# Kernel tuning notes

Measured on AMD Instinct MI355X. Metric: run time of the kernel, lower is better.

The kernel has to match this reference:

```python
import jax, jax.numpy as jnp
import numpy as np

TEACHER_TEMP = 0.07
STUDENT_TEMP = 0.1
N_SK_ITERS = 3
SK_EPS = 1e-8
KOLEO_EPS = 1e-8


def l2norm(x, eps=1e-12):
    # matches F.normalize(p=2, dim=-1): x / max(||x||, eps)
    n = jnp.linalg.norm(x, axis=-1, keepdims=True)
    return x / jnp.maximum(n, eps)


def sinkhorn_knopp(logits, temp):
    # logits: [M, K] -> doubly-stochastic-ish Q: [M, K]
    M = logits / temp
    M = M - jnp.max(M)
    Q = jnp.exp(M).T  # [K, M]
    for _ in range(N_SK_ITERS):
        Q = Q / (jnp.sum(Q, axis=1, keepdims=True) + SK_EPS)  # normalize over samples
        Q = Q / (jnp.sum(Q, axis=0, keepdims=True) + SK_EPS)  # normalize over prototypes
    return Q.T


def koleo_loss(x):
    # DINOv2 KoLeo: -mean(log(distance to nearest neighbor))
    x = l2norm(x, KOLEO_EPS)
    n = x.shape[0]
    dots = x @ x.T  # [K, K]
    dots = jnp.where(jnp.eye(n, dtype=bool), -1.0, dots)  # exclude self (fill diag with -1)
    nn_idx = jnp.argmax(dots, axis=1)
    d = jnp.linalg.norm(x - x[nn_idx], axis=-1)
    return -jnp.mean(jnp.log(d + KOLEO_EPS))


def setup_inputs() -> dict:
    key = jax.random.key(0)
    k1, k2, k3, k4 = jax.random.split(key, 4)
    B, N, D, K = 8, 1024, 768, 8192
    return {
        "teacher_patch_tokens": jax.random.normal(k1, (B, N, D), jnp.float32),
        "student_patch_tokens": jax.random.normal(k2, (B, N, D), jnp.float32),
        "token_masks": jax.random.randint(k3, (B, N), 0, 2) > 0,
        "proto_weight": jax.random.normal(k4, (K, D), jnp.float32) * 0.02,
    }


def reference(teacher_patch_tokens, student_patch_tokens, token_masks, proto_weight):
    B, N, D = teacher_patch_tokens.shape
    K = proto_weight.shape[0]

    t = l2norm(teacher_patch_tokens)  # [B,N,D]
    s = l2norm(student_patch_tokens)

    # prototype bank = bias-free linear: logits = x @ W^T
    t_logits = jnp.einsum('bnd,kd->bnk', t, proto_weight)  # [B,N,K]

    # Sinkhorn-Knopp targets (no grad)
    Q = jax.lax.stop_gradient(
        sinkhorn_knopp(t_logits.reshape(B * N, K), TEACHER_TEMP)
    ).reshape(B, N, K)

    t_logp = jax.nn.log_softmax(t_logits / TEACHER_TEMP, axis=-1)
    teacher_proto_loss = -jnp.sum(Q * t_logp) / (B * N)

    koleo = koleo_loss(l2norm(proto_weight))

    # Student cross-entropy on masked tokens. Dense-masked formulation:
    # computes the same mean over masked positions as boolean indexing.
    s_logits = jnp.einsum('bnd,kd->bnk', s, proto_weight)
    s_logp = jax.nn.log_softmax(s_logits / STUDENT_TEMP, axis=-1)
    per_token = -jnp.sum(Q * s_logp, axis=-1)  # [B,N]
    m = token_masks.astype(per_token.dtype)
    clustering_loss = jnp.sum(per_token * m) / jnp.maximum(jnp.sum(m), 1.0)

    return jnp.stack([clustering_loss, teacher_proto_loss, koleo])
```

## Files before the change

kernel.cpp:

```cpp
#include <hip/hip_runtime.h>
#include <stdint.h>

typedef unsigned short u16;
typedef __bf16 bf16x8 __attribute__((ext_vector_type(8)));
typedef float f32x4 __attribute__((ext_vector_type(4)));
typedef unsigned short u16x8 __attribute__((ext_vector_type(8)));
typedef unsigned short u16x4 __attribute__((ext_vector_type(4)));

#define SK_EPS 1e-8f
#define S_T 20.60992915555662f
#define S_S 14.426950408889634f
#define INV_TT 14.285714285714286f
#define INV_TS 10.0f

__device__ __forceinline__ float b2f(u16 u){ return __uint_as_float(((unsigned)u)<<16); }
__device__ __forceinline__ u16 f2b(float f){
  unsigned u = __float_as_uint(f);
  u += 0x7FFFu + ((u>>16)&1u);
  return (u16)(u>>16);
}
__device__ __forceinline__ unsigned encf(float x){ unsigned u=__float_as_uint(x); return (u&0x80000000u)? ~u : (u|0x80000000u); }
__device__ __forceinline__ float decf(unsigned u){ return (u&0x80000000u)? __uint_as_float(u&0x7FFFFFFFu) : __uint_as_float(~u); }

__device__ __forceinline__ void gload16(const void* g, void* l){
  __builtin_amdgcn_global_load_lds((const __attribute__((address_space(1))) void*)g,
                                   (__attribute__((address_space(3))) void*)l, 16, 0, 0);
}

__global__ __launch_bounds__(192) void norm_cast(const float* __restrict__ in, u16* __restrict__ out, int donorm){
  int row = blockIdx.x, tid = threadIdx.x;
  const float4* p = (const float4*)(in + (size_t)row*768);
  float4 v = p[tid];
  float ss = v.x*v.x + v.y*v.y + v.z*v.z + v.w*v.w;
  #pragma unroll
  for (int off=1; off<64; off<<=1) ss += __shfl_xor(ss, off);
  __shared__ float smem[3];
  int wv = tid>>6;
  if ((tid&63)==0) smem[wv] = ss;
  __syncthreads();
  float tot = smem[0]+smem[1]+smem[2];
  float scale = donorm ? (1.0f/fmaxf(sqrtf(tot), 1e-12f)) : 1.0f;
  u16x4 o;
  o[0]=f2b(v.x*scale); o[1]=f2b(v.y*scale); o[2]=f2b(v.z*scale); o[3]=f2b(v.w*scale);
  *(u16x4*)(out + (size_t)row*768 + tid*4) = o;
}

template<int MODE>
__global__ __launch_bounds__(256) void gemm_bt(
    const u16* __restrict__ A, const u16* __restrict__ B, int Ndim, int Kd,
    u16* __restrict__ Cout,
    const u16* __restrict__ Tl, const float* __restrict__ a3, const float* __restrict__ b3,
    float* __restrict__ sexp, float* __restrict__ sdot, unsigned* __restrict__ maxd)
{
  __shared__ __align__(16) u16 As[128*64];
  __shared__ __align__(16) u16 Bs[128*64];
  int tid = threadIdx.x, lane = tid & 63, wave = tid >> 6;
  int wr = wave >> 1, wc = wave & 1;
  int nbn = Ndim >> 7;
  int nwg = gridDim.x, cpx = nwg >> 3;
  int bid = blockIdx.x;
  int swz = (bid & 7)*cpx + (bid >> 3);
  int tm = swz / nbn, tn = swz % nbn;
  int m0 = tm<<7, n0 = tn<<7;

  const f32x4 fzero = {0.f,0.f,0.f,0.f};
  f32x4 acc[4][4];
  #pragma unroll
  for (int i=0;i<4;++i)
    #pragma unroll
    for (int j=0;j<4;++j) acc[i][j] = fzero;

  int srcRow = lane>>3;
  int srcCol = (((lane&7) ^ (lane>>3)) << 3);

  int nkt = Kd>>6;
  for (int kt=0; kt<nkt; ++kt){
    if (kt) __syncthreads();
    int k0 = kt<<6;
    #pragma unroll
    for (int c=0;c<4;++c){
      int chunk = (wave<<2)+c;
      int row = (chunk<<3) + srcRow;
      gload16(A + (size_t)(m0+row)*Kd + k0 + srcCol, (void*)(As + (chunk<<9)));
      gload16(B + (size_t)(n0+row)*Kd + k0 + srcCol, (void*)(Bs + (chunk<<9)));
    }
    asm volatile("s_waitcnt vmcnt(0)" ::: "memory");
    __syncthreads();
    #pragma unroll
    for (int ks=0; ks<2; ++ks){
      bf16x8 af[4], bfr[4];
      #pragma unroll
      for (int f=0; f<4; ++f){
        int rowA = (wr<<6)+(f<<4)+(lane&15);
        int idxA = ((rowA<<6) + (ks<<5) + ((lane>>4)<<3)) ^ ((lane&7)<<3);
        af[f] = *(const bf16x8*)(const void*)(As + idxA);
        int rowB = (wc<<6)+(f<<4)+(lane&15);
        int idxB = ((rowB<<6) + (ks<<5) + ((lane>>4)<<3)) ^ ((lane&7)<<3);
        bfr[f] = *(const bf16x8*)(const void*)(Bs + idxB);
      }
      #pragma unroll
      for (int fm=0;fm<4;++fm)
        #pragma unroll
        for (int fn=0;fn<4;++fn)
          acc[fm][fn] = __builtin_amdgcn_mfma_f32_16x16x32_bf16(af[fm], bfr[fn], acc[fm][fn], 0,0,0);
    }
  }

  if constexpr (MODE == 0){
    #pragma unroll
    for (int fm=0;fm<4;++fm)
      #pragma unroll
      for (int j=0;j<4;++j){
        size_t gr = (size_t)(m0 + (wr<<6)+(fm<<4)+((lane>>4)<<2)+j);
        #pragma unroll
        for (int fn=0;fn<4;++fn){
          int cl = (wc<<6)+(fn<<4)+(lane&15);
          Cout[gr*(size_t)Ndim + n0+cl] = f2b(acc[fm][fn][j]);
        }
      }
  } else if constexpr (MODE == 1){
    #pragma unroll
    for (int fm=0;fm<4;++fm)
      #pragma unroll
      for (int j=0;j<4;++j){
        size_t gr = (size_t)(m0 + (wr<<6)+(fm<<4)+((lane>>4)<<2)+j);
        float sx=0.f, sd=0.f;
        #pragma unroll
        for (int fn=0;fn<4;++fn){
          int cl = (wc<<6)+(fn<<4)+(lane&15);
          size_t gc = (size_t)(n0+cl);
          float v = acc[fm][fn][j];
          float tl = b2f(Tl[gr*(size_t)Ndim + gc]);
          sx += exp2f(v*S_S);
          sd += exp2f(tl*S_T)*a3[gc]*v;
        }
        #pragma unroll
        for (int off=1; off<16; off<<=1){ sx += __shfl_xor(sx,off); sd += __shfl_xor(sd,off); }
        if ((lane&15)==0){
          atomicAdd(&sexp[gr], sx);
          atomicAdd(&sdot[gr], b3[gr]*sd);
        }
      }
  } else {
    #pragma unroll
    for (int fm=0;fm<4;++fm)
      #pragma unroll
      for (int j=0;j<4;++j){
        size_t gr = (size_t)(m0 + (wr<<6)+(fm<<4)+((lane>>4)<<2)+j);
        float mx = -2.0f;
        #pragma unroll
        for (int fn=0;fn<4;++fn){
          int cl = (wc<<6)+(fn<<4)+(lane&15);
          size_t gc = (size_t)(n0+cl);
          float v = acc[fm][fn][j];
          if (gr != gc) mx = fmaxf(mx, v);
        }
        #pragma unroll
        for (int off=1; off<16; off<<=1) mx = fmaxf(mx, __shfl_xor(mx,off));
        if ((lane&15)==0) atomicMax(&maxd[gr], encf(mx));
      }
  }
}

__global__ __launch_bounds__(256) void sk_colsum(const u16* __restrict__ L, const float* __restrict__ bvec,
                                                 float* __restrict__ colOut, int Kc, int useb){
  int tid = threadIdx.x;
  int c0 = blockIdx.x*2048 + tid*8;
  int r0 = blockIdx.y*64;
  float acc[8] = {0.f,0.f,0.f,0.f,0.f,0.f,0.f,0.f};
  for (int r=r0; r<r0+64; ++r){
    u16x8 v = *(const u16x8*)(L + (size_t)r*Kc + c0);
    float bm = useb ? bvec[r] : 1.0f;
    #pragma unroll
    for (int i=0;i<8;++i) acc[i] += exp2f(b2f(v[i])*S_T)*bm;
  }
  #pragma unroll
  for (int i=0;i<8;++i) atomicAdd(&colOut[c0+i], acc[i]);
}

__global__ __launch_bounds__(256) void sk_rowsum(const u16* __restrict__ L, const float* __restrict__ avec,
    float* __restrict__ rowR, float* __restrict__ rowRE, float* __restrict__ rowT, int Kc, int mode){
  int m = blockIdx.x, tid = threadIdx.x;
  const u16* Lr = L + (size_t)m*Kc;
  float sR=0.f, sRE=0.f, sT=0.f;
  int nit = Kc/2048;
  for (int it=0; it<nit; ++it){
    int c = it*2048 + tid*8;
    u16x8 v = *(const u16x8*)(Lr + c);
    f32x4 alo = *(const f32x4*)(avec+c);
    f32x4 ahi = *(const f32x4*)(avec+c+4);
    #pragma unroll
    for (int i=0;i<8;++i){
      float l = b2f(v[i]);
      float E = exp2f(l*S_T);
      float a = (i<4)? alo[i] : ahi[i-4];
      float Ea = E*a;
      sR += Ea;
      if (mode&1) sRE += E;
      if (mode&2) sT += Ea*l;
    }
  }
  #pragma unroll
  for (int off=1; off<64; off<<=1){
    sR += __shfl_xor(sR,off);
    sRE += __shfl_xor(sRE,off);
    sT += __shfl_xor(sT,off);
  }
  __shared__ float red[3][4];
  int wv = tid>>6;
  if ((tid&63)==0){ red[0][wv]=sR; red[1][wv]=sRE; red[2][wv]=sT; }
  __syncthreads();
  if (tid==0){
    rowR[m] = red[0][0]+red[0][1]+red[0][2]+red[0][3];
    if (mode&1) rowRE[m] = red[1][0]+red[1][1]+red[1][2]+red[1][3];
    if (mode&2) rowT[m]  = red[2][0]+red[2][1]+red[2][2]+red[2][3];
  }
}

__global__ void upd_col(float* aV, float* colC, int K, int first){
  int k = blockIdx.x*256+threadIdx.x;
  if (k<K){
    float s = colC[k];
    float p = first ? 1.0f : aV[k];
    aV[k] = p/(p*s + SK_EPS);
    colC[k] = 0.0f;
  }
}
__global__ void upd_row(float* bV, const float* rowR, int M, int first){
  int m = blockIdx.x*256+threadIdx.x;
  if (m<M){
    float R = rowR[m];
    float p = first ? 1.0f : bV[m];
    bV[m] = p/(p*R + SK_EPS);
  }
}
__global__ void fin_rows(float* bV, const float* rowR, const float* rowRE, const float* rowT,
                         float* sumQ, float* ttok, int M){
  int m = blockIdx.x*256+threadIdx.x;
  if (m<M){
    float p = bV[m], R = rowR[m];
    float b3 = p/(p*R + SK_EPS);
    bV[m] = b3;
    float sq = b3*R;
    sumQ[m] = sq;
    ttok[m] = logf(rowRE[m])*sq - b3*rowT[m]*INV_TT;
  }
}

__global__ __launch_bounds__(1024) void finalize(const unsigned char* __restrict__ mask,
    const float* __restrict__ sexp, const float* __restrict__ sdot,
    const float* __restrict__ sumQ, const float* __restrict__ ttok,
    const unsigned* __restrict__ maxd, float* __restrict__ out, int M, int K){
  int tid = threadIdx.x;
  __shared__ int isBool;
  if (tid==0) isBool = 0;
  __syncthreads();
  int f = 0;
  for (int i=tid; i<M; i+=1024) if ((i&3) && mask[i]) f = 1;
  if (f) isBool = 1;
  __syncthreads();
  int ib = isBool;
  float cn=0.f, cc=0.f, ts=0.f, ks=0.f;
  for (int m=tid; m<M; m+=1024){
    int mk = ib ? (mask[m]!=0) : (((const int*)mask)[m]!=0);
    float pt = logf(sexp[m])*sumQ[m] - sdot[m]*INV_TS;
    if (mk){ cn += pt; cc += 1.0f; }
    ts += ttok[m];
  }
  for (int k=tid; k<K; k+=1024){
    float d = decf(maxd[k]);
    ks += logf(sqrtf(fmaxf(2.0f-2.0f*d, 0.0f)) + SK_EPS);
  }
  #pragma unroll
  for (int off=1; off<64; off<<=1){
    cn += __shfl_xor(cn,off); cc += __shfl_xor(cc,off);
    ts += __shfl_xor(ts,off); ks += __shfl_xor(ks,off);
  }
  __shared__ float red[4][16];
  int wv = tid>>6;
  if ((tid&63)==0){ red[0][wv]=cn; red[1][wv]=cc; red[2][wv]=ts; red[3][wv]=ks; }
  __syncthreads();
  if (tid==0){
    float CN=0,CC=0,TS=0,KS=0;
    for (int i=0;i<16;++i){ CN+=red[0][i]; CC+=red[1][i]; TS+=red[2][i]; KS+=red[3][i]; }
    out[0] = CN/fmaxf(CC,1.0f);
    out[1] = TS/(float)M;
    out[2] = -KS/(float)K;
  }
}

extern "C" void kernel_launch(void* const* d_in, const int* in_sizes, int n_in,
                              void* d_out, int out_size, void* d_ws, size_t ws_size,
                              hipStream_t stream){
  const float* teacher = (const float*)d_in[0];
  const float* student = (const float*)d_in[1];
  const unsigned char* mask = (const unsigned char*)d_in[2];
  const float* proto = (const float*)d_in[3];
  const int D = 768;
  const int M = in_sizes[0]/D;
  const int K = in_sizes[3]/D;
  float* out = (float*)d_out;

  char* ws = (char*)d_ws;
  size_t off = 0;
  auto alloc = [&](size_t bytes)->void*{ void* p = ws+off; off += (bytes+255)&~(size_t)255; return p; };
  u16* t_logits = (u16*)alloc((size_t)M*K*2);
  u16* t_hat    = (u16*)alloc((size_t)M*D*2);
  u16* s_hat    = (u16*)alloc((size_t)M*D*2);
  u16* w_bf     = (u16*)alloc((size_t)K*D*2);
  u16* w_hat    = (u16*)alloc((size_t)K*D*2);
  float* colC   = (float*)alloc((size_t)K*4);
  float* sexp   = (float*)alloc((size_t)M*4);
  float* sdot   = (float*)alloc((size_t)M*4);
  unsigned* maxd= (unsigned*)alloc((size_t)K*4);
  float* aV     = (float*)alloc((size_t)K*4);
  float* bV     = (float*)alloc((size_t)M*4);
  float* rowR   = (float*)alloc((size_t)M*4);
  float* rowRE  = (float*)alloc((size_t)M*4);
  float* rowT   = (float*)alloc((size_t)M*4);
  float* sumQ   = (float*)alloc((size_t)M*4);
  float* ttok   = (float*)alloc((size_t)M*4);

  hipMemsetAsync(colC, 0, (size_t)K*4, stream);
  hipMemsetAsync(sexp, 0, (size_t)M*4, stream);
  hipMemsetAsync(sdot, 0, (size_t)M*4, stream);
  hipMemsetAsync(maxd, 0, (size_t)K*4, stream);

  norm_cast<<<M, 192, 0, stream>>>(teacher, t_hat, 1);
  norm_cast<<<M, 192, 0, stream>>>(student, s_hat, 1);
  norm_cast<<<K, 192, 0, stream>>>(proto, w_bf, 0);
  norm_cast<<<K, 192, 0, stream>>>(proto, w_hat, 1);

  int nblk = (M/128)*(K/128);
  gemm_bt<0><<<nblk, 256, 0, stream>>>(t_hat, w_bf, K, D, t_logits,
                                       nullptr,nullptr,nullptr,nullptr,nullptr,nullptr);

  dim3 cgrid(K/2048, M/64);
  sk_colsum<<<cgrid, 256, 0, stream>>>(t_logits, nullptr, colC, K, 0);
  upd_col<<<(K+255)/256, 256, 0, stream>>>(aV, colC, K, 1);
  sk_rowsum<<<M, 256, 0, stream>>>(t_logits, aV, rowR, rowRE, rowT, K, 1);
  upd_row<<<(M+255)/256, 256, 0, stream>>>(bV, rowR, M, 1);
  sk_colsum<<<cgrid, 256, 0, stream>>>(t_logits, bV, colC, K, 1);
  upd_col<<<(K+255)/256, 256, 0, stream>>>(aV, colC, K, 0);
  sk_rowsum<<<M, 256, 0, stream>>>(t_logits, aV, rowR, rowRE, rowT, K, 0);
  upd_row<<<(M+255)/256, 256, 0, stream>>>(bV, rowR, M, 0);
  sk_colsum<<<cgrid, 256, 0, stream>>>(t_logits, bV, colC, K, 1);
  upd_col<<<(K+255)/256, 256, 0, stream>>>(aV, colC, K, 0);
  sk_rowsum<<<M, 256, 0, stream>>>(t_logits, aV, rowR, rowRE, rowT, K, 2);
  fin_rows<<<(M+255)/256, 256, 0, stream>>>(bV, rowR, rowRE, rowT, sumQ, ttok, M);

  gemm_bt<1><<<nblk, 256, 0, stream>>>(s_hat, w_bf, K, D, nullptr,
                                       t_logits, aV, bV, sexp, sdot, nullptr);
  gemm_bt<2><<<nblk, 256, 0, stream>>>(w_hat, w_hat, K, D, nullptr,
                                       nullptr,nullptr,nullptr,nullptr,nullptr, maxd);

  finalize<<<1, 1024, 0, stream>>>(mask, sexp, sdot, sumQ, ttok, maxd, out, M, K);
}
```

Measured before the change: 907.0 us.

## Use 256x256 double-buffered GEMM tiles and fuse first Sinkhorn column sum into epilogue

```diff
diff --git a/kernel.cpp b/kernel.cpp
--- a/kernel.cpp
+++ b/kernel.cpp
@@ -27,7 +27,8 @@
                                    (__attribute__((address_space(3))) void*)l, 16, 0, 0);
 }
 
-__global__ __launch_bounds__(192) void norm_cast(const float* __restrict__ in, u16* __restrict__ out, int donorm){
+__global__ __launch_bounds__(192) void norm_cast(const float* __restrict__ in, u16* __restrict__ out,
+                                                 u16* __restrict__ out2, int donorm){
   int row = blockIdx.x, tid = threadIdx.x;
   const float4* p = (const float4*)(in + (size_t)row*768);
   float4 v = p[tid];
@@ -41,42 +42,52 @@
   float tot = smem[0]+smem[1]+smem[2];
   float scale = donorm ? (1.0f/fmaxf(sqrtf(tot), 1e-12f)) : 1.0f;
   u16x4 o;
-  o[0]=f2b(v.x*scale); o[1]=f2b(v.y*scale); o[2]=f2b(v.z*scale); o[3]=f2b(v.w*scale);
-  *(u16x4*)(out + (size_t)row*768 + tid*4) = o;
+  o[0]=f2b(v.x); o[1]=f2b(v.y); o[2]=f2b(v.z); o[3]=f2b(v.w);
+  u16x4 on;
+  on[0]=f2b(v.x*scale); on[1]=f2b(v.y*scale); on[2]=f2b(v.z*scale); on[3]=f2b(v.w*scale);
+  if (out2){
+    *(u16x4*)(out  + (size_t)row*768 + tid*4) = o;
+    *(u16x4*)(out2 + (size_t)row*768 + tid*4) = on;
+  } else {
+    *(u16x4*)(out + (size_t)row*768 + tid*4) = donorm ? on : o;
+  }
 }
 
 template<int MODE>
-__global__ __launch_bounds__(256) void gemm_bt(
+__global__ __launch_bounds__(512, 2) void gemm_bt(
     const u16* __restrict__ A, const u16* __restrict__ B, int Ndim, int Kd,
-    u16* __restrict__ Cout,
+    u16* __restrict__ Cout, float* __restrict__ colC,
     const u16* __restrict__ Tl, const float* __restrict__ a3, const float* __restrict__ b3,
     float* __restrict__ sexp, float* __restrict__ sdot, unsigned* __restrict__ maxd)
 {
-  __shared__ __align__(16) u16 As[128*64];
-  __shared__ __align__(16) u16 Bs[128*64];
+  __shared__ __align__(16) u16 lds[65536];
   int tid = threadIdx.x, lane = tid & 63, wave = tid >> 6;
-  int wr = wave >> 1, wc = wave & 1;
-  int nbn = Ndim >> 7;
-  int nwg = gridDim.x, cpx = nwg >> 3;
-  int bid = blockIdx.x;
-  int swz = (bid & 7)*cpx + (bid >> 3);
-  int tm = swz / nbn, tn = swz % nbn;
-  int m0 = tm<<7, n0 = tn<<7;
+  int wr = wave >> 2, wc = wave & 3;
+
+  int bid = blockIdx.x, tm, tn;
+  if (gridDim.x == 1024){
+    int xcd = bid & 7, local = bid >> 3;
+    int g = local >> 4, w = local & 15;
+    tn = g*4 + (w & 3);
+    tm = xcd*4 + (w >> 2);
+  } else { int nbn = Ndim >> 8; tm = bid / nbn; tn = bid % nbn; }
+  int m0 = tm << 8, n0 = tn << 8;
 
   const f32x4 fzero = {0.f,0.f,0.f,0.f};
-  f32x4 acc[4][4];
+  f32x4 acc[8][4];
   #pragma unroll
-  for (int i=0;i<4;++i)
+  for (int i=0;i<8;++i)
     #pragma unroll
     for (int j=0;j<4;++j) acc[i][j] = fzero;
 
   int srcRow = lane>>3;
   int srcCol = (((lane&7) ^ (lane>>3)) << 3);
 
-  int nkt = Kd>>6;
-  for (int kt=0; kt<nkt; ++kt){
-    if (kt) __syncthreads();
-    int k0 = kt<<6;
+  const int nkt = Kd >> 6;
+  auto stage = [&](int p, int kt){
+    int k0 = kt << 6;
+    u16* As = lds + p*32768;
+    u16* Bs = As + 16384;
     #pragma unroll
     for (int c=0;c<4;++c){
       int chunk = (wave<<2)+c;
@@ -84,53 +95,91 @@
       gload16(A + (size_t)(m0+row)*Kd + k0 + srcCol, (void*)(As + (chunk<<9)));
       gload16(B + (size_t)(n0+row)*Kd + k0 + srcCol, (void*)(Bs + (chunk<<9)));
     }
-    asm volatile("s_waitcnt vmcnt(0)" ::: "memory");
-    __syncthreads();
+  };
+
+  stage(0, 0);
+  int p = 0;
+  for (int kt=0; kt<nkt; ++kt){
+    if (kt+1 < nkt){
+      stage(p^1, kt+1);
+      asm volatile("s_waitcnt vmcnt(8)" ::: "memory");
+    } else {
+      asm volatile("s_waitcnt vmcnt(0)" ::: "memory");
+    }
+    __builtin_amdgcn_s_barrier();
+    __builtin_amdgcn_sched_barrier(0);
+    const u16* As = lds + p*32768;
+    const u16* Bs = As + 16384;
     #pragma unroll
     for (int ks=0; ks<2; ++ks){
-      bf16x8 af[4], bfr[4];
-      #pragma unroll
-      for (int f=0; f<4; ++f){
-        int rowA = (wr<<6)+(f<<4)+(lane&15);
+      bf16x8 af[8], bfr[4];
+      #pragma unroll
+      for (int f=0; f<8; ++f){
+        int rowA = (wr<<7)+(f<<4)+(lane&15);
         int idxA = ((rowA<<6) + (ks<<5) + ((lane>>4)<<3)) ^ ((lane&7)<<3);
         af[f] = *(const bf16x8*)(const void*)(As + idxA);
+      }
+      #pragma unroll
+      for (int f=0; f<4; ++f){
         int rowB = (wc<<6)+(f<<4)+(lane&15);
         int idxB = ((rowB<<6) + (ks<<5) + ((lane>>4)<<3)) ^ ((lane&7)<<3);
         bfr[f] = *(const bf16x8*)(const void*)(Bs + idxB);
       }
       #pragma unroll
-      for (int fm=0;fm<4;++fm)
+      for (int fm=0;fm<8;++fm)
         #pragma unroll
         for (int fn=0;fn<4;++fn)
           acc[fm][fn] = __builtin_amdgcn_mfma_f32_16x16x32_bf16(af[fm], bfr[fn], acc[fm][fn], 0,0,0);
     }
+    __builtin_amdgcn_sched_barrier(0);
+    __builtin_amdgcn_s_barrier();
+    p ^= 1;
   }
 
   if constexpr (MODE == 0){
-    #pragma unroll
-    for (int fm=0;fm<4;++fm)
+    float cs[4] = {0.f,0.f,0.f,0.f};
+    #pragma unroll
+    for (int fm=0;fm<8;++fm)
       #pragma unroll
       for (int j=0;j<4;++j){
-        size_t gr = (size_t)(m0 + (wr<<6)+(fm<<4)+((lane>>4)<<2)+j);
+        size_t gr = (size_t)(m0 + (wr<<7)+(fm<<4)+((lane>>4)<<2)+j);
         #pragma unroll
         for (int fn=0;fn<4;++fn){
           int cl = (wc<<6)+(fn<<4)+(lane&15);
-          Cout[gr*(size_t)Ndim + n0+cl] = f2b(acc[fm][fn][j]);
+          u16 hb = f2b(acc[fm][fn][j]);
+          Cout[gr*(size_t)Ndim + n0+cl] = hb;
+          cs[fn] += exp2f(b2f(hb)*S_T);
         }
       }
+    #pragma unroll
+    for (int fn=0;fn<4;++fn){
+      float v = cs[fn];
+      v += __shfl_xor(v,16); v += __shfl_xor(v,32);
+      if (lane < 16) atomicAdd(&colC[n0 + (wc<<6)+(fn<<4)+lane], v);
+    }
   } else if constexpr (MODE == 1){
     #pragma unroll
-    for (int fm=0;fm<4;++fm)
+    for (int i=0;i<16;++i){
+      int wch = (wave<<4) + i;
+      int grow = (wch<<1) + (lane>>5);
+      int gcol = (lane&31)<<3;
+      gload16(Tl + (size_t)(m0+grow)*Ndim + n0 + gcol, (void*)(lds + (wch<<9)));
+    }
+    asm volatile("s_waitcnt vmcnt(0)" ::: "memory");
+    __syncthreads();
+    #pragma unroll
+    for (int fm=0;fm<8;++fm)
       #pragma unroll
       for (int j=0;j<4;++j){
-        size_t gr = (size_t)(m0 + (wr<<6)+(fm<<4)+((lane>>4)<<2)+j);
+        int lrow = (wr<<7)+(fm<<4)+((lane>>4)<<2)+j;
+        size_t gr = (size_t)(m0 + lrow);
         float sx=0.f, sd=0.f;
         #pragma unroll
         for (int fn=0;fn<4;++fn){
           int cl = (wc<<6)+(fn<<4)+(lane&15);
           size_t gc = (size_t)(n0+cl);
           float v = acc[fm][fn][j];
-          float tl = b2f(Tl[gr*(size_t)Ndim + gc]);
+          float tl = b2f(lds[(size_t)lrow*256 + cl]);
           sx += exp2f(v*S_S);
           sd += exp2f(tl*S_T)*a3[gc]*v;
         }
@@ -143,10 +192,10 @@
       }
   } else {
     #pragma unroll
-    for (int fm=0;fm<4;++fm)
+    for (int fm=0;fm<8;++fm)
       #pragma unroll
       for (int j=0;j<4;++j){
-        size_t gr = (size_t)(m0 + (wr<<6)+(fm<<4)+((lane>>4)<<2)+j);
+        size_t gr = (size_t)(m0 + (wr<<7)+(fm<<4)+((lane>>4)<<2)+j);
         float mx = -2.0f;
         #pragma unroll
         for (int fn=0;fn<4;++fn){
@@ -326,17 +375,15 @@
   hipMemsetAsync(sdot, 0, (size_t)M*4, stream);
   hipMemsetAsync(maxd, 0, (size_t)K*4, stream);
 
-  norm_cast<<<M, 192, 0, stream>>>(teacher, t_hat, 1);
-  norm_cast<<<M, 192, 0, stream>>>(student, s_hat, 1);
-  norm_cast<<<K, 192, 0, stream>>>(proto, w_bf, 0);
-  norm_cast<<<K, 192, 0, stream>>>(proto, w_hat, 1);
-
-  int nblk = (M/128)*(K/128);
-  gemm_bt<0><<<nblk, 256, 0, stream>>>(t_hat, w_bf, K, D, t_logits,
+  norm_cast<<<M, 192, 0, stream>>>(teacher, t_hat, nullptr, 1);
+  norm_cast<<<M, 192, 0, stream>>>(student, s_hat, nullptr, 1);
+  norm_cast<<<K, 192, 0, stream>>>(proto, w_bf, w_hat, 1);
+
+  int nblk = (M/256)*(K/256);
+  gemm_bt<0><<<nblk, 512, 0, stream>>>(t_hat, w_bf, K, D, t_logits, colC,
                                        nullptr,nullptr,nullptr,nullptr,nullptr,nullptr);
 
   dim3 cgrid(K/2048, M/64);
-  sk_colsum<<<cgrid, 256, 0, stream>>>(t_logits, nullptr, colC, K, 0);
   upd_col<<<(K+255)/256, 256, 0, stream>>>(aV, colC, K, 1);
   sk_rowsum<<<M, 256, 0, stream>>>(t_logits, aV, rowR, rowRE, rowT, K, 1);
   upd_row<<<(M+255)/256, 256, 0, stream>>>(bV, rowR, M, 1);
@@ -349,9 +396,9 @@
   sk_rowsum<<<M, 256, 0, stream>>>(t_logits, aV, rowR, rowRE, rowT, K, 2);
   fin_rows<<<(M+255)/256, 256, 0, stream>>>(bV, rowR, rowRE, rowT, sumQ, ttok, M);
 
-  gemm_bt<1><<<nblk, 256, 0, stream>>>(s_hat, w_bf, K, D, nullptr,
+  gemm_bt<1><<<nblk, 512, 0, stream>>>(s_hat, w_bf, K, D, nullptr, nullptr,
                                        t_logits, aV, bV, sexp, sdot, nullptr);
-  gemm_bt<2><<<nblk, 256, 0, stream>>>(w_hat, w_hat, K, D, nullptr,
+  gemm_bt<2><<<nblk, 512, 0, stream>>>(w_hat, w_hat, K, D, nullptr, nullptr,
                                        nullptr,nullptr,nullptr,nullptr,nullptr, maxd);
 
   finalize<<<1, 1024, 0, stream>>>(mask, sexp, sdot, sumQ, ttok, maxd, out, M, K);
```

Result: faster. 755.4 us (-16.7%).

## Fuse first Sinkhorn column-sum into teacher GEMM epilogue and merge proto casts

Applied to the files above, without the earlier changes.

```diff
diff --git a/kernel.cpp b/kernel.cpp
--- a/kernel.cpp
+++ b/kernel.cpp
@@ -27,7 +27,8 @@
                                    (__attribute__((address_space(3))) void*)l, 16, 0, 0);
 }
 
-__global__ __launch_bounds__(192) void norm_cast(const float* __restrict__ in, u16* __restrict__ out, int donorm){
+__global__ __launch_bounds__(192) void norm_cast(const float* __restrict__ in, u16* __restrict__ out,
+                                                 u16* __restrict__ out2, int donorm){
   int row = blockIdx.x, tid = threadIdx.x;
   const float4* p = (const float4*)(in + (size_t)row*768);
   float4 v = p[tid];
@@ -41,14 +42,21 @@
   float tot = smem[0]+smem[1]+smem[2];
   float scale = donorm ? (1.0f/fmaxf(sqrtf(tot), 1e-12f)) : 1.0f;
   u16x4 o;
-  o[0]=f2b(v.x*scale); o[1]=f2b(v.y*scale); o[2]=f2b(v.z*scale); o[3]=f2b(v.w*scale);
-  *(u16x4*)(out + (size_t)row*768 + tid*4) = o;
+  o[0]=f2b(v.x); o[1]=f2b(v.y); o[2]=f2b(v.z); o[3]=f2b(v.w);
+  u16x4 on;
+  on[0]=f2b(v.x*scale); on[1]=f2b(v.y*scale); on[2]=f2b(v.z*scale); on[3]=f2b(v.w*scale);
+  if (out2){
+    *(u16x4*)(out  + (size_t)row*768 + tid*4) = o;
+    *(u16x4*)(out2 + (size_t)row*768 + tid*4) = on;
+  } else {
+    *(u16x4*)(out + (size_t)row*768 + tid*4) = donorm ? on : o;
+  }
 }
 
 template<int MODE>
 __global__ __launch_bounds__(256) void gemm_bt(
     const u16* __restrict__ A, const u16* __restrict__ B, int Ndim, int Kd,
-    u16* __restrict__ Cout,
+    u16* __restrict__ Cout, float* __restrict__ colC,
     const u16* __restrict__ Tl, const float* __restrict__ a3, const float* __restrict__ b3,
     float* __restrict__ sexp, float* __restrict__ sdot, unsigned* __restrict__ maxd)
 {
@@ -56,11 +64,14 @@
   __shared__ __align__(16) u16 Bs[128*64];
   int tid = threadIdx.x, lane = tid & 63, wave = tid >> 6;
   int wr = wave >> 1, wc = wave & 1;
-  int nbn = Ndim >> 7;
-  int nwg = gridDim.x, cpx = nwg >> 3;
-  int bid = blockIdx.x;
-  int swz = (bid & 7)*cpx + (bid >> 3);
-  int tm = swz / nbn, tn = swz % nbn;
+
+  int bid = blockIdx.x, tm, tn;
+  if (gridDim.x == 4096){
+    int xcd = bid & 7, local = bid >> 3;
+    int g = local >> 6, w = local & 63;
+    tm = xcd*8 + (w >> 3);
+    tn = g*8 + (w & 7);
+  } else { int nbn = Ndim >> 7; tm = bid / nbn; tn = bid % nbn; }
   int m0 = tm<<7, n0 = tn<<7;
 
   const f32x4 fzero = {0.f,0.f,0.f,0.f};
@@ -107,6 +118,7 @@
   }
 
   if constexpr (MODE == 0){
+    float cs[4] = {0.f,0.f,0.f,0.f};
     #pragma unroll
     for (int fm=0;fm<4;++fm)
       #pragma unroll
@@ -115,9 +127,17 @@
         #pragma unroll
         for (int fn=0;fn<4;++fn){
           int cl = (wc<<6)+(fn<<4)+(lane&15);
-          Cout[gr*(size_t)Ndim + n0+cl] = f2b(acc[fm][fn][j]);
+          u16 hb = f2b(acc[fm][fn][j]);
+          Cout[gr*(size_t)Ndim + n0+cl] = hb;
+          cs[fn] += exp2f(b2f(hb)*S_T);
         }
       }
+    #pragma unroll
+    for (int fn=0;fn<4;++fn){
+      float v = cs[fn];
+      v += __shfl_xor(v,16); v += __shfl_xor(v,32);
+      if (lane < 16) atomicAdd(&colC[n0 + (wc<<6)+(fn<<4)+lane], v);
+    }
   } else if constexpr (MODE == 1){
     #pragma unroll
     for (int fm=0;fm<4;++fm)
@@ -326,17 +346,15 @@
   hipMemsetAsync(sdot, 0, (size_t)M*4, stream);
   hipMemsetAsync(maxd, 0, (size_t)K*4, stream);
 
-  norm_cast<<<M, 192, 0, stream>>>(teacher, t_hat, 1);
-  norm_cast<<<M, 192, 0, stream>>>(student, s_hat, 1);
-  norm_cast<<<K, 192, 0, stream>>>(proto, w_bf, 0);
-  norm_cast<<<K, 192, 0, stream>>>(proto, w_hat, 1);
+  norm_cast<<<M, 192, 0, stream>>>(teacher, t_hat, nullptr, 1);
+  norm_cast<<<M, 192, 0, stream>>>(student, s_hat, nullptr, 1);
+  norm_cast<<<K, 192, 0, stream>>>(proto, w_bf, w_hat, 1);
 
   int nblk = (M/128)*(K/128);
-  gemm_bt<0><<<nblk, 256, 0, stream>>>(t_hat, w_bf, K, D, t_logits,
+  gemm_bt<0><<<nblk, 256, 0, stream>>>(t_hat, w_bf, K, D, t_logits, colC,
                                        nullptr,nullptr,nullptr,nullptr,nullptr,nullptr);
 
   dim3 cgrid(K/2048, M/64);
-  sk_colsum<<<cgrid, 256, 0, stream>>>(t_logits, nullptr, colC, K, 0);
   upd_col<<<(K+255)/256, 256, 0, stream>>>(aV, colC, K, 1);
   sk_rowsum<<<M, 256, 0, stream>>>(t_logits, aV, rowR, rowRE, rowT, K, 1);
   upd_row<<<(M+255)/256, 256, 0, stream>>>(bV, rowR, M, 1);
@@ -349,9 +367,9 @@
   sk_rowsum<<<M, 256, 0, stream>>>(t_logits, aV, rowR, rowRE, rowT, K, 2);
   fin_rows<<<(M+255)/256, 256, 0, stream>>>(bV, rowR, rowRE, rowT, sumQ, ttok, M);
 
-  gemm_bt<1><<<nblk, 256, 0, stream>>>(s_hat, w_bf, K, D, nullptr,
+  gemm_bt<1><<<nblk, 256, 0, stream>>>(s_hat, w_bf, K, D, nullptr, nullptr,
                                        t_logits, aV, bV, sexp, sdot, nullptr);
-  gemm_bt<2><<<nblk, 256, 0, stream>>>(w_hat, w_hat, K, D, nullptr,
+  gemm_bt<2><<<nblk, 256, 0, stream>>>(w_hat, w_hat, K, D, nullptr, nullptr,
                                        nullptr,nullptr,nullptr,nullptr,nullptr, maxd);
 
   finalize<<<1, 1024, 0, stream>>>(mask, sexp, sdot, sumQ, ttok, maxd, out, M, K);
```

Result: faster. 733.5 us (-19.1%).
